# Optimization experiments

Measured on AMD Instinct MI355X. Metric: run time of the kernel, lower is better.

The kernel has to match this reference:

```python
import jax, jax.numpy as jnp
import numpy as np

DIMS = 2048
Q_HEADS = 32
K_HEADS = 8
HEAD_DIM = DIMS // Q_HEADS  # 64
KV_DIM = K_HEADS * HEAD_DIM  # 512
B, S, IN_DIM = 2, 2048, 2048


def setup_inputs() -> dict:
    key = jax.random.key(0)
    ks = jax.random.split(key, 11)
    sc_in = 1.0 / np.sqrt(IN_DIM)
    sc_out = 1.0 / np.sqrt(DIMS)
    return {
        "q": jax.random.normal(ks[0], (B, S, IN_DIM), jnp.float32),
        "k": jax.random.normal(ks[1], (B, S, IN_DIM), jnp.float32),
        "v": jax.random.normal(ks[2], (B, S, IN_DIM), jnp.float32),
        "Wq": jax.random.normal(ks[3], (IN_DIM, DIMS), jnp.float32) * sc_in,
        "bq": jnp.zeros((DIMS,), jnp.float32),
        "Wk": jax.random.normal(ks[4], (IN_DIM, KV_DIM), jnp.float32) * sc_in,
        "bk": jnp.zeros((KV_DIM,), jnp.float32),
        "Wv": jax.random.normal(ks[5], (IN_DIM, KV_DIM), jnp.float32) * sc_in,
        "bv": jnp.zeros((KV_DIM,), jnp.float32),
        "Wo": jax.random.normal(ks[6], (DIMS, IN_DIM), jnp.float32) * sc_out,
        "bo": jnp.zeros((IN_DIM,), jnp.float32),
    }


def reference(q, k, v, Wq, bq, Wk, bk, Wv, bv, Wo, bo):
    rep = Q_HEADS // K_HEADS
    # projections
    qx = (q @ Wq + bq).reshape(B, S, Q_HEADS, HEAD_DIM)
    kx = (k @ Wk + bk).reshape(B, S, K_HEADS, HEAD_DIM)
    vx = (v @ Wv + bv).reshape(B, S, K_HEADS, HEAD_DIM)
    # repeat kv heads to match q heads (matches kx.repeat(rep, axis=-2))
    kx = jnp.repeat(kx, rep, axis=-2)
    vx = jnpp_repeat(vx, rep) if False else jnp.repeat(vx, rep, axis=-2)
    # [B, H, S, D]
    qx = jnp.einsum('bshd->bhsd', qx)
    kx = jnp.einsum('bshd->bhsd', kx)
    vx = jnp.einsum('bshd->bhsd', vx)
    scores = jnp.einsum('bhqd,bhkd->bhqk', qx, kx) / jnp.sqrt(
        jnp.asarray(HEAD_DIM, qx.dtype))
    scores = jax.nn.softmax(scores, axis=-1)
    out = jnp.einsum('bhqk,bhkd->bhqd', scores, vx)
    out = jnp.einsum('bhsd->bshd', out).reshape(B, S, DIMS)
    return out @ Wo + bo
```

## Files before the change

kernel.cpp:

```cpp
#include <hip/hip_runtime.h>
#include <cstdint>
#include <cstddef>

typedef _Float16 half8   __attribute__((ext_vector_type(8)));
typedef _Float16 half4_t __attribute__((ext_vector_type(4)));
typedef __fp16   fp16x2  __attribute__((ext_vector_type(2)));
typedef float    f32x4   __attribute__((ext_vector_type(4)));

typedef __attribute__((address_space(1))) const void GV;
typedef __attribute__((address_space(3))) void LV;

__device__ __forceinline__ void gl_lds16(const _Float16* g, _Float16* l) {
    __builtin_amdgcn_global_load_lds((GV*)g, (LV*)l, 16, 0, 0);
}

#define BB    2
#define SS    2048
#define INDIM 2048
#define DIMS_ 2048
#define QH    32
#define KH_   8
#define HD    64
#define KVD   512
#define RWS   4096

#define QSCALE (0.125f * 1.44269504088896340736f)

__global__ void cast_f16_3(const float* __restrict__ a, const float* __restrict__ b,
                           const float* __restrict__ c,
                           _Float16* __restrict__ oa, _Float16* __restrict__ ob,
                           _Float16* __restrict__ oc) {
    const float* in  = (blockIdx.y == 0) ? a : (blockIdx.y == 1) ? b : c;
    _Float16*    out = (blockIdx.y == 0) ? oa : (blockIdx.y == 1) ? ob : oc;
    int i = (blockIdx.x * 256 + threadIdx.x) * 8;
    const float4* p = (const float4*)(in + i);
    float4 x = p[0], y = p[1];
    half8 h;
    h[0]=(_Float16)x.x; h[1]=(_Float16)x.y; h[2]=(_Float16)x.z; h[3]=(_Float16)x.w;
    h[4]=(_Float16)y.x; h[5]=(_Float16)y.y; h[6]=(_Float16)y.z; h[7]=(_Float16)y.w;
    *(half8*)(out + i) = h;
}

__global__ void transpose_cast4(const float* __restrict__ in0, _Float16* __restrict__ out0,
                                const float* __restrict__ in1, _Float16* __restrict__ out1,
                                const float* __restrict__ in2, _Float16* __restrict__ out2,
                                const float* __restrict__ in3, _Float16* __restrict__ out3,
                                int R, int C01, int C23) {
    const int z = blockIdx.z;
    const float* in; _Float16* out; int C;
    if (z == 0)      { in = in0; out = out0; C = C01; }
    else if (z == 1) { in = in1; out = out1; C = C01; }
    else if (z == 2) { in = in2; out = out2; C = C23; }
    else             { in = in3; out = out3; C = C23; }
    int c0 = blockIdx.x * 32;
    if (c0 >= C) return;
    __shared__ float t[32][33];
    int r0 = blockIdx.y * 32;
    int tx = threadIdx.x, ty = threadIdx.y;
    for (int i = ty; i < 32; i += 8)
        t[i][tx] = in[(size_t)(r0 + i) * C + c0 + tx];
    __syncthreads();
    for (int i = ty; i < 32; i += 8)
        out[(size_t)(c0 + i) * R + r0 + tx] = (_Float16)t[tx][i];
}

__global__ __launch_bounds__(256) void gemm_qkv(
    const _Float16* __restrict__ q16, const _Float16* __restrict__ k16,
    const _Float16* __restrict__ v16,
    const _Float16* __restrict__ WqT, const _Float16* __restrict__ WkT,
    const _Float16* __restrict__ WvT,
    const float* __restrict__ bq, const float* __restrict__ bk,
    const float* __restrict__ bv,
    _Float16* __restrict__ qx, _Float16* __restrict__ kx,
    _Float16* __restrict__ vtg)
{
    const int bid = blockIdx.x;
    const _Float16* A; const _Float16* Bt; const float* bias;
    int bn, bm, N, mode; float scale;
    if (bid < 512)      { mode = 0; A = q16; Bt = WqT; bias = bq; N = 2048;
                          bn = bid & 15; bm = bid >> 4; scale = QSCALE; }
    else if (bid < 640) { int t = bid - 512; mode = 1; A = k16; Bt = WkT; bias = bk;
                          N = 512; bn = t & 3; bm = t >> 2; scale = 1.0f; }
    else                { int t = bid - 640; mode = 2; A = v16; Bt = WvT; bias = bv;
                          N = 512; bn = t & 3; bm = t >> 2; scale = 1.0f; }
    const int K = 2048;

    const int tid = threadIdx.x;
    const int wave = tid >> 6, lane = tid & 63, quad = lane >> 4, l15 = lane & 15;
    const int wm = wave & 1, wn = wave >> 1;

    __shared__ __align__(16) _Float16 As[2][128 * 32];
    __shared__ __align__(16) _Float16 Bs[2][128 * 32];

    f32x4 acc[4][4] = {};

    const _Float16* Agb = A  + (size_t)(bm * 128) * K;
    const _Float16* Bgb = Bt + (size_t)(bn * 128) * K;

#define QKV_STAGE(T, BUF)                                                     \
    {                                                                         \
        const _Float16* Ag = Agb + (T) * 32;                                  \
        const _Float16* Bg = Bgb + (T) * 32;                                  \
        _Float16* Ad = &As[BUF][0];                                           \
        _Float16* Bd = &Bs[BUF][0];                                           \
        _Pragma("unroll")                                                     \
        for (int i_ = 0; i_ < 2; ++i_) {                                      \
            int f_ = i_ * 256 + tid;                                          \
            gl_lds16(Ag + (size_t)(f_ >> 2) * K + (f_ & 3) * 8,               \
                     Ad + (size_t)(i_ * 256 + (tid & 192)) * 8);              \
            gl_lds16(Bg + (size_t)(f_ >> 2) * K + (f_ & 3) * 8,               \
                     Bd + (size_t)(i_ * 256 + (tid & 192)) * 8);              \
        }                                                                     \
    }

    QKV_STAGE(0, 0);

    for (int kt = 0; kt < K / 32; ++kt) {
        const int cur = kt & 1;
        if (kt < K / 32 - 1) {
            QKV_STAGE(kt + 1, cur ^ 1);
            asm volatile("s_waitcnt vmcnt(4)" ::: "memory");
        } else {
            asm volatile("s_waitcnt vmcnt(0)" ::: "memory");
        }
        __builtin_amdgcn_s_barrier();

        half8 af[4], bf[4];
#pragma unroll
        for (int i = 0; i < 4; ++i)
            af[i] = *(const half8*)(&As[cur][0] + (wm * 64 + i * 16 + l15) * 32 + quad * 8);
#pragma unroll
        for (int j = 0; j < 4; ++j)
            bf[j] = *(const half8*)(&Bs[cur][0] + (wn * 64 + j * 16 + l15) * 32 + quad * 8);
        __builtin_amdgcn_s_setprio(1);
#pragma unroll
        for (int i = 0; i < 4; ++i)
#pragma unroll
            for (int j = 0; j < 4; ++j)
                acc[i][j] = __builtin_amdgcn_mfma_f32_16x16x32_f16(af[i], bf[j], acc[i][j], 0, 0, 0);
        __builtin_amdgcn_s_setprio(0);
        __builtin_amdgcn_s_barrier();
    }

    const int row0 = bm * 128 + wm * 64;
    const int col0 = bn * 128 + wn * 64;
    if (mode < 2) {
        _Float16* out = mode ? kx : qx;
#pragma unroll
        for (int j = 0; j < 4; ++j) {
            int col = col0 + j * 16 + l15;
            float bv_ = bias[col];
#pragma unroll
            for (int i = 0; i < 4; ++i)
#pragma unroll
                for (int r = 0; r < 4; ++r) {
                    int row = row0 + i * 16 + quad * 4 + r;
                    out[(size_t)row * N + col] = (_Float16)((acc[i][j][r] + bv_) * scale);
                }
        }
    } else {
#pragma unroll
        for (int j = 0; j < 4; ++j) {
            int c = col0 + j * 16 + l15;
            int kh = c >> 6, d = c & 63;
            float bv_ = bias[c];
#pragma unroll
            for (int i = 0; i < 4; ++i) {
                int row = row0 + i * 16 + quad * 4;
                int bb2 = row >> 11, s = row & 2047;
                half4_t hp;
#pragma unroll
                for (int r = 0; r < 4; ++r) hp[r] = (_Float16)(acc[i][j][r] + bv_);
                *(half4_t*)(vtg + ((size_t)(bb2 * KH_ + kh) * HD + d) * SS + s) = hp;
            }
        }
    }
}

__global__ __launch_bounds__(256) void gemm_oproj(
    const _Float16* __restrict__ A, const _Float16* __restrict__ Bt,
    const float* __restrict__ bias, float* __restrict__ Cf)
{
    const int N = 2048, K = 2048;
    const int bn = blockIdx.x, bm = blockIdx.y;
    const int tid = threadIdx.x;
    const int wave = tid >> 6, lane = tid & 63, quad = lane >> 4, l15 = lane & 15;
    const int wm = wave & 1, wn = wave >> 1;

    __shared__ __align__(16) _Float16 As[2][128 * 32];
    __shared__ __align__(16) _Float16 Bs[2][128 * 32];

    f32x4 acc[4][4] = {};

    const _Float16* Agb = A  + (size_t)(bm * 128) * K;
    const _Float16* Bgb = Bt + (size_t)(bn * 128) * K;

    QKV_STAGE(0, 0);

    for (int kt = 0; kt < K / 32; ++kt) {
        const int cur = kt & 1;
        if (kt < K / 32 - 1) {
            QKV_STAGE(kt + 1, cur ^ 1);
            asm volatile("s_waitcnt vmcnt(4)" ::: "memory");
        } else {
            asm volatile("s_waitcnt vmcnt(0)" ::: "memory");
        }
        __builtin_amdgcn_s_barrier();

        half8 af[4], bf[4];
#pragma unroll
        for (int i = 0; i < 4; ++i)
            af[i] = *(const half8*)(&As[cur][0] + (wm * 64 + i * 16 + l15) * 32 + quad * 8);
#pragma unroll
        for (int j = 0; j < 4; ++j)
            bf[j] = *(const half8*)(&Bs[cur][0] + (wn * 64 + j * 16 + l15) * 32 + quad * 8);
        __builtin_amdgcn_s_setprio(1);
#pragma unroll
        for (int i = 0; i < 4; ++i)
#pragma unroll
            for (int j = 0; j < 4; ++j)
                acc[i][j] = __builtin_amdgcn_mfma_f32_16x16x32_f16(af[i], bf[j], acc[i][j], 0, 0, 0);
        __builtin_amdgcn_s_setprio(0);
        __builtin_amdgcn_s_barrier();
    }

    const int row0 = bm * 128 + wm * 64;
    const int col0 = bn * 128 + wn * 64;
#pragma unroll
    for (int j = 0; j < 4; ++j) {
        int col = col0 + j * 16 + l15;
        float bv_ = bias[col];
#pragma unroll
        for (int i = 0; i < 4; ++i)
#pragma unroll
            for (int r = 0; r < 4; ++r) {
                int row = row0 + i * 16 + quad * 4 + r;
                Cf[(size_t)row * N + col] = acc[i][j][r] + bv_;
            }
    }
}

__global__ __launch_bounds__(256, 4) void attn_fused(
    const _Float16* __restrict__ qx, const _Float16* __restrict__ kx,
    const _Float16* __restrict__ vt, _Float16* __restrict__ o16)
{
    const int qt = blockIdx.x;
    const int bh = blockIdx.y;
    const int bb = bh >> 5, h = bh & 31, kh = h >> 2;
    const int tid = threadIdx.x;
    const int w = tid >> 6, lane = tid & 63, quad = lane >> 4, l15 = lane & 15;

    __shared__ __align__(16) _Float16 Ks[64 * 64];
    __shared__ __align__(16) _Float16 Vs[64 * 64];
    __shared__ __align__(16) _Float16 Ps[4][32 * 72];

    const size_t qrow0 = (size_t)bb * SS + (size_t)qt * 128 + w * 32;
    half8 qf[2][2];
#pragma unroll
    for (int nb = 0; nb < 2; ++nb)
#pragma unroll
        for (int kk = 0; kk < 2; ++kk)
            qf[nb][kk] = *(const half8*)(qx + (qrow0 + nb * 16 + l15) * DIMS_
                                            + h * HD + kk * 32 + quad * 8);

    half8 vone;
#pragma unroll
    for (int i = 0; i < 8; ++i) vone[i] = (_Float16)1.0f;

    f32x4 ob[2][4] = {};
    f32x4 lacc[2] = {};

    const _Float16* kbase = kx + (size_t)bb * SS * KVD + kh * HD;
    const _Float16* vbase = vt + (size_t)(bb * KH_ + kh) * HD * SS;
    _Float16* Pw = &Ps[w][0];

    const int srowlo = lane >> 3;
    const int scol   = ((lane & 7) ^ srowlo) * 8;

    for (int kt = 0; kt < SS / 64; ++kt) {
        __syncthreads();
#pragma unroll
        for (int i = 0; i < 2; ++i) {
            int row = w * 16 + i * 8 + srowlo;
            gl_lds16(kbase + (size_t)(kt * 64 + row) * KVD + scol,
                     Ks + (w * 16 + i * 8) * 64);
            gl_lds16(vbase + (size_t)row * SS + kt * 64 + scol,
                     Vs + (w * 16 + i * 8) * 64);
        }
        __syncthreads();

#pragma unroll
        for (int mk = 0; mk < 4; ++mk) {
            f32x4 st4[2] = {};
#pragma unroll
            for (int kk = 0; kk < 2; ++kk) {
                half8 ka = *(const half8*)(Ks + (mk * 16 + l15) * 64
                                              + (((kk * 4 + quad) ^ (l15 & 7)) * 8));
                __builtin_amdgcn_s_setprio(1);
#pragma unroll
                for (int nb = 0; nb < 2; ++nb)
                    st4[nb] = __builtin_amdgcn_mfma_f32_16x16x32_f16(
                        ka, qf[nb][kk], st4[nb], 0, 0, 0);
                __builtin_amdgcn_s_setprio(0);
            }
#pragma unroll
            for (int nb = 0; nb < 2; ++nb) {
                float p0 = __builtin_amdgcn_exp2f(st4[nb][0]);
                float p1 = __builtin_amdgcn_exp2f(st4[nb][1]);
                float p2 = __builtin_amdgcn_exp2f(st4[nb][2]);
                float p3 = __builtin_amdgcn_exp2f(st4[nb][3]);
                fp16x2 lo = __builtin_amdgcn_cvt_pkrtz(p0, p1);
                fp16x2 hi = __builtin_amdgcn_cvt_pkrtz(p2, p3);
                half4_t hp;
                hp[0] = (_Float16)lo[0]; hp[1] = (_Float16)lo[1];
                hp[2] = (_Float16)hi[0]; hp[3] = (_Float16)hi[1];
                *(half4_t*)(Pw + (nb * 16 + l15) * 72 + mk * 16 + quad * 4) = hp;
            }
        }

#pragma unroll
        for (int kk = 0; kk < 2; ++kk) {
            half8 pa[2], vb[4];
#pragma unroll
            for (int mb = 0; mb < 2; ++mb)
                pa[mb] = *(const half8*)(Pw + (mb * 16 + l15) * 72 + kk * 32 + quad * 8);
#pragma unroll
            for (int nd = 0; nd < 4; ++nd)
                vb[nd] = *(const half8*)(Vs + (nd * 16 + l15) * 64
                                            + (((kk * 4 + quad) ^ (l15 & 7)) * 8));
            __builtin_amdgcn_s_setprio(1);
#pragma unroll
            for (int mb = 0; mb < 2; ++mb) {
#pragma unroll
                for (int nd = 0; nd < 4; ++nd)
                    ob[mb][nd] = __builtin_amdgcn_mfma_f32_16x16x32_f16(
                        pa[mb], vb[nd], ob[mb][nd], 0, 0, 0);
                lacc[mb] = __builtin_amdgcn_mfma_f32_16x16x32_f16(
                    pa[mb], vone, lacc[mb], 0, 0, 0);
            }
            __builtin_amdgcn_s_setprio(0);
        }
    }

#pragma unroll
    for (int mb = 0; mb < 2; ++mb)
#pragma unroll
        for (int r = 0; r < 4; ++r) {
            float rl = __builtin_amdgcn_rcpf(lacc[mb][r]);
            size_t row = qrow0 + mb * 16 + quad * 4 + r;
#pragma unroll
            for (int nd = 0; nd < 4; ++nd)
                o16[row * DIMS_ + h * HD + nd * 16 + l15] =
                    (_Float16)(ob[mb][nd][r] * rl);
        }
}

extern "C" void kernel_launch(void* const* d_in, const int* in_sizes, int n_in,
                              void* d_out, int out_size, void* d_ws, size_t ws_size,
                              hipStream_t stream) {
    const float* q  = (const float*)d_in[0];
    const float* k  = (const float*)d_in[1];
    const float* v  = (const float*)d_in[2];
    const float* Wq = (const float*)d_in[3];
    const float* bq = (const float*)d_in[4];
    const float* Wk = (const float*)d_in[5];
    const float* bk = (const float*)d_in[6];
    const float* Wv = (const float*)d_in[7];
    const float* bv = (const float*)d_in[8];
    const float* Wo = (const float*)d_in[9];
    const float* bo = (const float*)d_in[10];

    char* ws = (char*)d_ws;
    _Float16* q16  = (_Float16*)ws;  ws += (size_t)RWS * INDIM * 2;
    _Float16* k16  = (_Float16*)ws;  ws += (size_t)RWS * INDIM * 2;
    _Float16* v16  = (_Float16*)ws;  ws += (size_t)RWS * INDIM * 2;
    _Float16* qx16 = (_Float16*)ws;  ws += (size_t)RWS * DIMS_ * 2;
    _Float16* kx16 = (_Float16*)ws;  ws += (size_t)RWS * KVD * 2;
    _Float16* o16  = (_Float16*)ws;  ws += (size_t)RWS * DIMS_ * 2;
    _Float16* WqT  = (_Float16*)ws;  ws += (size_t)DIMS_ * INDIM * 2;
    _Float16* WkT  = (_Float16*)ws;  ws += (size_t)KVD * INDIM * 2;
    _Float16* WvT  = (_Float16*)ws;  ws += (size_t)KVD * INDIM * 2;
    _Float16* WoT  = (_Float16*)ws;  ws += (size_t)INDIM * DIMS_ * 2;
    _Float16* vtg  = (_Float16*)ws;  ws += (size_t)BB * KH_ * HD * SS * 2;

    const int nAct = RWS * INDIM;
    cast_f16_3<<<dim3(nAct / (256 * 8), 3), 256, 0, stream>>>(q, k, v, q16, k16, v16);

    transpose_cast4<<<dim3(DIMS_ / 32, INDIM / 32, 4), dim3(32, 8), 0, stream>>>(
        Wq, WqT, Wo, WoT, Wk, WkT, Wv, WvT, INDIM, DIMS_, KVD);

    gemm_qkv<<<768, 256, 0, stream>>>(q16, k16, v16, WqT, WkT, WvT,
                                      bq, bk, bv, qx16, kx16, vtg);

    attn_fused<<<dim3(SS / 128, BB * QH), 256, 0, stream>>>(qx16, kx16, vtg, o16);

    gemm_oproj<<<dim3(INDIM / 128, RWS / 128), 256, 0, stream>>>(
        o16, WoT, bo, (float*)d_out);
}
```

Measured before the change: 404.3 us.

## Use 256x256 tiles with 8 waves and swizzled LDS for QKV GEMM

```diff
diff --git a/kernel.cpp b/kernel.cpp
--- a/kernel.cpp
+++ b/kernel.cpp
@@ -64,7 +64,7 @@
         out[(size_t)(c0 + i) * R + r0 + tx] = (_Float16)t[tx][i];
 }
 
-__global__ __launch_bounds__(256) void gemm_qkv(
+__global__ __launch_bounds__(512, 2) void gemm_qkv256(
     const _Float16* __restrict__ q16, const _Float16* __restrict__ k16,
     const _Float16* __restrict__ v16,
     const _Float16* __restrict__ WqT, const _Float16* __restrict__ WkT,
@@ -74,103 +74,139 @@
     _Float16* __restrict__ qx, _Float16* __restrict__ kx,
     _Float16* __restrict__ vtg)
 {
-    const int bid = blockIdx.x;
+    const int K = 2048;
+    const int wg = blockIdx.x;
+    const int wgid = (wg & 7) * 24 + (wg >> 3);
+
     const _Float16* A; const _Float16* Bt; const float* bias;
-    int bn, bm, N, mode; float scale;
-    if (bid < 512)      { mode = 0; A = q16; Bt = WqT; bias = bq; N = 2048;
-                          bn = bid & 15; bm = bid >> 4; scale = QSCALE; }
-    else if (bid < 640) { int t = bid - 512; mode = 1; A = k16; Bt = WkT; bias = bk;
-                          N = 512; bn = t & 3; bm = t >> 2; scale = 1.0f; }
-    else                { int t = bid - 640; mode = 2; A = v16; Bt = WvT; bias = bv;
-                          N = 512; bn = t & 3; bm = t >> 2; scale = 1.0f; }
-    const int K = 2048;
+    int bm, bn, mode; float scale;
+    if (wgid < 128)      { mode = 0; A = q16; Bt = WqT; bias = bq;
+                           bm = wgid >> 3; bn = wgid & 7; scale = QSCALE; }
+    else if (wgid < 160) { int t = wgid - 128; mode = 1; A = k16; Bt = WkT; bias = bk;
+                           bm = t >> 1; bn = t & 1; scale = 1.0f; }
+    else                 { int t = wgid - 160; mode = 2; A = v16; Bt = WvT; bias = bv;
+                           bm = t >> 1; bn = t & 1; scale = 1.0f; }
 
     const int tid = threadIdx.x;
-    const int wave = tid >> 6, lane = tid & 63, quad = lane >> 4, l15 = lane & 15;
-    const int wm = wave & 1, wn = wave >> 1;
-
-    __shared__ __align__(16) _Float16 As[2][128 * 32];
-    __shared__ __align__(16) _Float16 Bs[2][128 * 32];
-
-    f32x4 acc[4][4] = {};
-
-    const _Float16* Agb = A  + (size_t)(bm * 128) * K;
-    const _Float16* Bgb = Bt + (size_t)(bn * 128) * K;
-
-#define QKV_STAGE(T, BUF)                                                     \
-    {                                                                         \
-        const _Float16* Ag = Agb + (T) * 32;                                  \
-        const _Float16* Bg = Bgb + (T) * 32;                                  \
-        _Float16* Ad = &As[BUF][0];                                           \
-        _Float16* Bd = &Bs[BUF][0];                                           \
-        _Pragma("unroll")                                                     \
-        for (int i_ = 0; i_ < 2; ++i_) {                                      \
-            int f_ = i_ * 256 + tid;                                          \
-            gl_lds16(Ag + (size_t)(f_ >> 2) * K + (f_ & 3) * 8,               \
-                     Ad + (size_t)(i_ * 256 + (tid & 192)) * 8);              \
-            gl_lds16(Bg + (size_t)(f_ >> 2) * K + (f_ & 3) * 8,               \
-                     Bd + (size_t)(i_ * 256 + (tid & 192)) * 8);              \
-        }                                                                     \
-    }
-
-    QKV_STAGE(0, 0);
-
-    for (int kt = 0; kt < K / 32; ++kt) {
+    const int w = tid >> 6, lane = tid & 63, quad = lane >> 4, l15 = lane & 15;
+    const int wm = w >> 2, wn = w & 3;
+
+    __shared__ __align__(16) _Float16 As[2][16384];
+    __shared__ __align__(16) _Float16 Bs[2][16384];
+
+    int offs[4];
+#pragma unroll
+    for (int hr = 0; hr < 4; ++hr) {
+        int x = (hr >> 1) * 16384 + (hr & 1) * 8192 + tid * 16;
+        int L = x ^ (((x >> 9) & 1) << 5);
+        offs[hr] = (L >> 7) * K + ((L & 127) >> 1);
+    }
+    const _Float16* Ag = A  + (size_t)(bm * 256) * K;
+    const _Float16* Bg = Bt + (size_t)(bn * 256) * K;
+
+#define STAGE_A(BUF, KT)                                                     \
+    _Pragma("unroll")                                                        \
+    for (int hr_ = 0; hr_ < 4; ++hr_)                                        \
+        gl_lds16(Ag + (KT) * 64 + offs[hr_],                                 \
+                 &As[BUF][(hr_ >> 1) * 8192 + (hr_ & 1) * 4096 + w * 512]);
+#define STAGE_B(BUF, KT)                                                     \
+    _Pragma("unroll")                                                        \
+    for (int hr_ = 0; hr_ < 4; ++hr_)                                        \
+        gl_lds16(Bg + (KT) * 64 + offs[hr_],                                 \
+                 &Bs[BUF][(hr_ >> 1) * 8192 + (hr_ & 1) * 4096 + w * 512]);
+
+#define RD_A(BUF, MH)                                                        \
+    _Pragma("unroll")                                                        \
+    for (int i_ = 0; i_ < 4; ++i_) {                                         \
+        int row_ = wm * 128 + (MH) * 64 + i_ * 16 + l15;                     \
+        int rsw_ = (row_ & 4) << 2;                                          \
+        _Pragma("unroll")                                                    \
+        for (int kk_ = 0; kk_ < 2; ++kk_)                                    \
+            af[i_][kk_] = *(const half8*)(&As[BUF][row_ * 64 +               \
+                                    ((kk_ * 32 + quad * 8) ^ rsw_)]);        \
+    }
+#define RD_B(BUF, NH, DST)                                                   \
+    _Pragma("unroll")                                                        \
+    for (int j_ = 0; j_ < 2; ++j_) {                                         \
+        int row_ = wn * 64 + (NH) * 32 + j_ * 16 + l15;                      \
+        int rsw_ = (row_ & 4) << 2;                                          \
+        _Pragma("unroll")                                                    \
+        for (int kk_ = 0; kk_ < 2; ++kk_)                                    \
+            DST[j_][kk_] = *(const half8*)(&Bs[BUF][row_ * 64 +              \
+                                    ((kk_ * 32 + quad * 8) ^ rsw_)]);        \
+    }
+#define QUAD16(MH, NH, BF)                                                   \
+    __builtin_amdgcn_s_setprio(1);                                           \
+    _Pragma("unroll")                                                        \
+    for (int i_ = 0; i_ < 4; ++i_)                                           \
+        _Pragma("unroll")                                                    \
+        for (int j_ = 0; j_ < 2; ++j_)                                       \
+            _Pragma("unroll")                                                \
+            for (int kk_ = 0; kk_ < 2; ++kk_)                                \
+                acc[(MH) * 4 + i_][(NH) * 2 + j_] =                          \
+                    __builtin_amdgcn_mfma_f32_16x16x32_f16(                  \
+                        af[i_][kk_], BF[j_][kk_],                            \
+                        acc[(MH) * 4 + i_][(NH) * 2 + j_], 0, 0, 0);         \
+    __builtin_amdgcn_s_setprio(0);
+
+    f32x4 acc[8][4] = {};
+    half8 af[4][2], bf0[2][2], bf1[2][2];
+
+    STAGE_A(0, 0); STAGE_B(0, 0);
+    asm volatile("s_waitcnt vmcnt(0)" ::: "memory");
+    __builtin_amdgcn_s_barrier();
+
+    for (int kt = 0; kt < 32; ++kt) {
         const int cur = kt & 1;
-        if (kt < K / 32 - 1) {
-            QKV_STAGE(kt + 1, cur ^ 1);
-            asm volatile("s_waitcnt vmcnt(4)" ::: "memory");
-        } else {
-            asm volatile("s_waitcnt vmcnt(0)" ::: "memory");
-        }
-        __builtin_amdgcn_s_barrier();
-
-        half8 af[4], bf[4];
-#pragma unroll
-        for (int i = 0; i < 4; ++i)
-            af[i] = *(const half8*)(&As[cur][0] + (wm * 64 + i * 16 + l15) * 32 + quad * 8);
-#pragma unroll
-        for (int j = 0; j < 4; ++j)
-            bf[j] = *(const half8*)(&Bs[cur][0] + (wn * 64 + j * 16 + l15) * 32 + quad * 8);
-        __builtin_amdgcn_s_setprio(1);
-#pragma unroll
-        for (int i = 0; i < 4; ++i)
-#pragma unroll
-            for (int j = 0; j < 4; ++j)
-                acc[i][j] = __builtin_amdgcn_mfma_f32_16x16x32_f16(af[i], bf[j], acc[i][j], 0, 0, 0);
-        __builtin_amdgcn_s_setprio(0);
-        __builtin_amdgcn_s_barrier();
-    }
-
-    const int row0 = bm * 128 + wm * 64;
-    const int col0 = bn * 128 + wn * 64;
+        RD_A(cur, 0); RD_B(cur, 0, bf0);
+        if (kt < 31) { STAGE_A(cur ^ 1, kt + 1); }
+        __builtin_amdgcn_s_barrier();
+        QUAD16(0, 0, bf0);
+        __builtin_amdgcn_s_barrier();
+        RD_B(cur, 1, bf1);
+        if (kt < 31) { STAGE_B(cur ^ 1, kt + 1); }
+        __builtin_amdgcn_s_barrier();
+        QUAD16(0, 1, bf1);
+        __builtin_amdgcn_s_barrier();
+        RD_A(cur, 1);
+        __builtin_amdgcn_s_barrier();
+        QUAD16(1, 0, bf0);
+        __builtin_amdgcn_s_barrier();
+        QUAD16(1, 1, bf1);
+        asm volatile("s_waitcnt vmcnt(0)" ::: "memory");
+        __builtin_amdgcn_s_barrier();
+    }
+
+    const int row0 = bm * 256 + wm * 128;
+    const int col0 = bn * 256 + wn * 64;
     if (mode < 2) {
         _Float16* out = mode ? kx : qx;
-#pragma unroll
-        for (int j = 0; j < 4; ++j) {
-            int col = col0 + j * 16 + l15;
+        const int N = mode ? 512 : 2048;
+#pragma unroll
+        for (int jj = 0; jj < 4; ++jj) {
+            int col = col0 + jj * 16 + l15;
             float bv_ = bias[col];
 #pragma unroll
-            for (int i = 0; i < 4; ++i)
+            for (int mf = 0; mf < 8; ++mf)
 #pragma unroll
                 for (int r = 0; r < 4; ++r) {
-                    int row = row0 + i * 16 + quad * 4 + r;
-                    out[(size_t)row * N + col] = (_Float16)((acc[i][j][r] + bv_) * scale);
+                    int row = row0 + mf * 16 + quad * 4 + r;
+                    out[(size_t)row * N + col] = (_Float16)((acc[mf][jj][r] + bv_) * scale);
                 }
         }
     } else {
 #pragma unroll
-        for (int j = 0; j < 4; ++j) {
-            int c = col0 + j * 16 + l15;
+        for (int jj = 0; jj < 4; ++jj) {
+            int c = col0 + jj * 16 + l15;
             int kh = c >> 6, d = c & 63;
             float bv_ = bias[c];
 #pragma unroll
-            for (int i = 0; i < 4; ++i) {
-                int row = row0 + i * 16 + quad * 4;
+            for (int mf = 0; mf < 8; ++mf) {
+                int row = row0 + mf * 16 + quad * 4;
                 int bb2 = row >> 11, s = row & 2047;
                 half4_t hp;
 #pragma unroll
-                for (int r = 0; r < 4; ++r) hp[r] = (_Float16)(acc[i][j][r] + bv_);
+                for (int r = 0; r < 4; ++r) hp[r] = (_Float16)(acc[mf][jj][r] + bv_);
                 *(half4_t*)(vtg + ((size_t)(bb2 * KH_ + kh) * HD + d) * SS + s) = hp;
             }
         }
@@ -187,41 +223,37 @@
     const int wave = tid >> 6, lane = tid & 63, quad = lane >> 4, l15 = lane & 15;
     const int wm = wave & 1, wn = wave >> 1;
 
-    __shared__ __align__(16) _Float16 As[2][128 * 32];
-    __shared__ __align__(16) _Float16 Bs[2][128 * 32];
+    __shared__ __align__(16) _Float16 As[128 * 32];
+    __shared__ __align__(16) _Float16 Bs[128 * 32];
 
     f32x4 acc[4][4] = {};
 
-    const _Float16* Agb = A  + (size_t)(bm * 128) * K;
-    const _Float16* Bgb = Bt + (size_t)(bn * 128) * K;
-
-    QKV_STAGE(0, 0);
-
     for (int kt = 0; kt < K / 32; ++kt) {
-        const int cur = kt & 1;
-        if (kt < K / 32 - 1) {
-            QKV_STAGE(kt + 1, cur ^ 1);
-            asm volatile("s_waitcnt vmcnt(4)" ::: "memory");
-        } else {
-            asm volatile("s_waitcnt vmcnt(0)" ::: "memory");
-        }
-        __builtin_amdgcn_s_barrier();
+        __syncthreads();
+        const _Float16* Ag = A  + (size_t)(bm * 128) * K + kt * 32;
+        const _Float16* Bg = Bt + (size_t)(bn * 128) * K + kt * 32;
+#pragma unroll
+        for (int i = 0; i < 2; ++i) {
+            int f = i * 256 + tid;
+            gl_lds16(Ag + (size_t)(f >> 2) * K + (f & 3) * 8,
+                     As + (size_t)(i * 256 + (tid & 192)) * 8);
+            gl_lds16(Bg + (size_t)(f >> 2) * K + (f & 3) * 8,
+                     Bs + (size_t)(i * 256 + (tid & 192)) * 8);
+        }
+        __syncthreads();
 
         half8 af[4], bf[4];
 #pragma unroll
         for (int i = 0; i < 4; ++i)
-            af[i] = *(const half8*)(&As[cur][0] + (wm * 64 + i * 16 + l15) * 32 + quad * 8);
+            af[i] = *(const half8*)(As + (wm * 64 + i * 16 + l15) * 32 + quad * 8);
 #pragma unroll
         for (int j = 0; j < 4; ++j)
-            bf[j] = *(const half8*)(&Bs[cur][0] + (wn * 64 + j * 16 + l15) * 32 + quad * 8);
-        __builtin_amdgcn_s_setprio(1);
+            bf[j] = *(const half8*)(Bs + (wn * 64 + j * 16 + l15) * 32 + quad * 8);
 #pragma unroll
         for (int i = 0; i < 4; ++i)
 #pragma unroll
             for (int j = 0; j < 4; ++j)
                 acc[i][j] = __builtin_amdgcn_mfma_f32_16x16x32_f16(af[i], bf[j], acc[i][j], 0, 0, 0);
-        __builtin_amdgcn_s_setprio(0);
-        __builtin_amdgcn_s_barrier();
     }
 
     const int row0 = bm * 128 + wm * 64;
@@ -389,8 +421,8 @@
     transpose_cast4<<<dim3(DIMS_ / 32, INDIM / 32, 4), dim3(32, 8), 0, stream>>>(
         Wq, WqT, Wo, WoT, Wk, WkT, Wv, WvT, INDIM, DIMS_, KVD);
 
-    gemm_qkv<<<768, 256, 0, stream>>>(q16, k16, v16, WqT, WkT, WvT,
-                                      bq, bk, bv, qx16, kx16, vtg);
+    gemm_qkv256<<<192, 512, 0, stream>>>(q16, k16, v16, WqT, WkT, WvT,
+                                         bq, bk, bv, qx16, kx16, vtg);
 
     attn_fused<<<dim3(SS / 128, BB * QH), 256, 0, stream>>>(qx16, kx16, vtg, o16);
 
```

Result: faster. 383.8 us (-5.1%).

## Use single-buffered 64-wide K tiles with XOR-swizzled LDS in projection GEMMs

Applied to the files above, without the earlier changes.

```diff
diff --git a/kernel.cpp b/kernel.cpp
--- a/kernel.cpp
+++ b/kernel.cpp
@@ -89,57 +89,52 @@
     const int wave = tid >> 6, lane = tid & 63, quad = lane >> 4, l15 = lane & 15;
     const int wm = wave & 1, wn = wave >> 1;
 
-    __shared__ __align__(16) _Float16 As[2][128 * 32];
-    __shared__ __align__(16) _Float16 Bs[2][128 * 32];
+    __shared__ __align__(16) _Float16 As[128 * 64];
+    __shared__ __align__(16) _Float16 Bs[128 * 64];
 
     f32x4 acc[4][4] = {};
 
-    const _Float16* Agb = A  + (size_t)(bm * 128) * K;
-    const _Float16* Bgb = Bt + (size_t)(bn * 128) * K;
-
-#define QKV_STAGE(T, BUF)                                                     \
-    {                                                                         \
-        const _Float16* Ag = Agb + (T) * 32;                                  \
-        const _Float16* Bg = Bgb + (T) * 32;                                  \
-        _Float16* Ad = &As[BUF][0];                                           \
-        _Float16* Bd = &Bs[BUF][0];                                           \
-        _Pragma("unroll")                                                     \
-        for (int i_ = 0; i_ < 2; ++i_) {                                      \
-            int f_ = i_ * 256 + tid;                                          \
-            gl_lds16(Ag + (size_t)(f_ >> 2) * K + (f_ & 3) * 8,               \
-                     Ad + (size_t)(i_ * 256 + (tid & 192)) * 8);              \
-            gl_lds16(Bg + (size_t)(f_ >> 2) * K + (f_ & 3) * 8,               \
-                     Bd + (size_t)(i_ * 256 + (tid & 192)) * 8);              \
-        }                                                                     \
-    }
-
-    QKV_STAGE(0, 0);
-
-    for (int kt = 0; kt < K / 32; ++kt) {
-        const int cur = kt & 1;
-        if (kt < K / 32 - 1) {
-            QKV_STAGE(kt + 1, cur ^ 1);
-            asm volatile("s_waitcnt vmcnt(4)" ::: "memory");
-        } else {
-            asm volatile("s_waitcnt vmcnt(0)" ::: "memory");
-        }
-        __builtin_amdgcn_s_barrier();
-
-        half8 af[4], bf[4];
-#pragma unroll
-        for (int i = 0; i < 4; ++i)
-            af[i] = *(const half8*)(&As[cur][0] + (wm * 64 + i * 16 + l15) * 32 + quad * 8);
-#pragma unroll
-        for (int j = 0; j < 4; ++j)
-            bf[j] = *(const half8*)(&Bs[cur][0] + (wn * 64 + j * 16 + l15) * 32 + quad * 8);
-        __builtin_amdgcn_s_setprio(1);
-#pragma unroll
-        for (int i = 0; i < 4; ++i)
-#pragma unroll
-            for (int j = 0; j < 4; ++j)
-                acc[i][j] = __builtin_amdgcn_mfma_f32_16x16x32_f16(af[i], bf[j], acc[i][j], 0, 0, 0);
-        __builtin_amdgcn_s_setprio(0);
-        __builtin_amdgcn_s_barrier();
+    const int srow = tid >> 3;
+    const int scol = (((lane & 7) ^ ((lane >> 3) & 7))) * 8;
+
+    for (int kt = 0; kt < K / 64; ++kt) {
+        __syncthreads();
+        const _Float16* Ag = A  + (size_t)(bm * 128) * K + kt * 64;
+        const _Float16* Bg = Bt + (size_t)(bn * 128) * K + kt * 64;
+#pragma unroll
+        for (int Lm = 0; Lm < 4; ++Lm) {
+            gl_lds16(Ag + (size_t)(Lm * 32 + srow) * K + scol,
+                     As + Lm * 2048 + wave * 512);
+            gl_lds16(Bg + (size_t)(Lm * 32 + srow) * K + scol,
+                     Bs + Lm * 2048 + wave * 512);
+        }
+        __syncthreads();
+
+        half8 af[4][2], bf[4][2];
+#pragma unroll
+        for (int i = 0; i < 4; ++i) {
+            int row = wm * 64 + i * 16 + l15;
+#pragma unroll
+            for (int kk = 0; kk < 2; ++kk)
+                af[i][kk] = *(const half8*)(As + row * 64
+                                              + (((kk * 4 + quad) ^ (l15 & 7)) * 8));
+        }
+#pragma unroll
+        for (int j = 0; j < 4; ++j) {
+            int row = wn * 64 + j * 16 + l15;
+#pragma unroll
+            for (int kk = 0; kk < 2; ++kk)
+                bf[j][kk] = *(const half8*)(Bs + row * 64
+                                              + (((kk * 4 + quad) ^ (l15 & 7)) * 8));
+        }
+#pragma unroll
+        for (int kk = 0; kk < 2; ++kk)
+#pragma unroll
+            for (int i = 0; i < 4; ++i)
+#pragma unroll
+                for (int j = 0; j < 4; ++j)
+                    acc[i][j] = __builtin_amdgcn_mfma_f32_16x16x32_f16(
+                        af[i][kk], bf[j][kk], acc[i][j], 0, 0, 0);
     }
 
     const int row0 = bm * 128 + wm * 64;
@@ -187,41 +182,52 @@
     const int wave = tid >> 6, lane = tid & 63, quad = lane >> 4, l15 = lane & 15;
     const int wm = wave & 1, wn = wave >> 1;
 
-    __shared__ __align__(16) _Float16 As[2][128 * 32];
-    __shared__ __align__(16) _Float16 Bs[2][128 * 32];
+    __shared__ __align__(16) _Float16 As[128 * 64];
+    __shared__ __align__(16) _Float16 Bs[128 * 64];
 
     f32x4 acc[4][4] = {};
 
-    const _Float16* Agb = A  + (size_t)(bm * 128) * K;
-    const _Float16* Bgb = Bt + (size_t)(bn * 128) * K;
-
-    QKV_STAGE(0, 0);
-
-    for (int kt = 0; kt < K / 32; ++kt) {
-        const int cur = kt & 1;
-        if (kt < K / 32 - 1) {
-            QKV_STAGE(kt + 1, cur ^ 1);
-            asm volatile("s_waitcnt vmcnt(4)" ::: "memory");
-        } else {
-            asm volatile("s_waitcnt vmcnt(0)" ::: "memory");
-        }
-        __builtin_amdgcn_s_barrier();
-
-        half8 af[4], bf[4];
-#pragma unroll
-        for (int i = 0; i < 4; ++i)
-            af[i] = *(const half8*)(&As[cur][0] + (wm * 64 + i * 16 + l15) * 32 + quad * 8);
-#pragma unroll
-        for (int j = 0; j < 4; ++j)
-            bf[j] = *(const half8*)(&Bs[cur][0] + (wn * 64 + j * 16 + l15) * 32 + quad * 8);
-        __builtin_amdgcn_s_setprio(1);
-#pragma unroll
-        for (int i = 0; i < 4; ++i)
-#pragma unroll
-            for (int j = 0; j < 4; ++j)
-                acc[i][j] = __builtin_amdgcn_mfma_f32_16x16x32_f16(af[i], bf[j], acc[i][j], 0, 0, 0);
-        __builtin_amdgcn_s_setprio(0);
-        __builtin_amdgcn_s_barrier();
+    const int srow = tid >> 3;
+    const int scol = (((lane & 7) ^ ((lane >> 3) & 7))) * 8;
+
+    for (int kt = 0; kt < K / 64; ++kt) {
+        __syncthreads();
+        const _Float16* Ag = A  + (size_t)(bm * 128) * K + kt * 64;
+        const _Float16* Bg = Bt + (size_t)(bn * 128) * K + kt * 64;
+#pragma unroll
+        for (int Lm = 0; Lm < 4; ++Lm) {
+            gl_lds16(Ag + (size_t)(Lm * 32 + srow) * K + scol,
+                     As + Lm * 2048 + wave * 512);
+            gl_lds16(Bg + (size_t)(Lm * 32 + srow) * K + scol,
+                     Bs + Lm * 2048 + wave * 512);
+        }
+        __syncthreads();
+
+        half8 af[4][2], bf[4][2];
+#pragma unroll
+        for (int i = 0; i < 4; ++i) {
+            int row = wm * 64 + i * 16 + l15;
+#pragma unroll
+            for (int kk = 0; kk < 2; ++kk)
+                af[i][kk] = *(const half8*)(As + row * 64
+                                              + (((kk * 4 + quad) ^ (l15 & 7)) * 8));
+        }
+#pragma unroll
+        for (int j = 0; j < 4; ++j) {
+            int row = wn * 64 + j * 16 + l15;
+#pragma unroll
+            for (int kk = 0; kk < 2; ++kk)
+                bf[j][kk] = *(const half8*)(Bs + row * 64
+                                              + (((kk * 4 + quad) ^ (l15 & 7)) * 8));
+        }
+#pragma unroll
+        for (int kk = 0; kk < 2; ++kk)
+#pragma unroll
+            for (int i = 0; i < 4; ++i)
+#pragma unroll
+                for (int j = 0; j < 4; ++j)
+                    acc[i][j] = __builtin_amdgcn_mfma_f32_16x16x32_f16(
+                        af[i][kk], bf[j][kk], acc[i][j], 0, 0, 0);
     }
 
     const int row0 = bm * 128 + wm * 64;
```

New measurement: 379.8 us. -6.0%, faster.
